# Kernel tuning notes

Hardware: AMD Instinct MI355X
Metric: run time of the kernel (lower is better)

Reference implementation:

```python
import jax, jax.numpy as jnp
import numpy as np
import math

SR = 24000
NH = 100      # num_harmonics
NF = 5        # num_formants
HID = 128
TWO_PI = 2.0 * math.pi


def conv1d(x, w, b, groups=1):
    # x: [B,C,T], w: [O, C//groups, K] (torch OIH layout), 'same' padding
    pad = (w.shape[-1] - 1) // 2
    y = jax.lax.conv_general_dilated(
        x, w, window_strides=(1,), padding=[(pad, pad)],
        dimension_numbers=('NCH', 'OIH', 'NCH'), feature_group_count=groups)
    return y + b[None, :, None]


def lrelu(x):
    return jnp.where(x >= 0, x, 0.1 * x)


def interp_linear(x, L):
    # torch F.interpolate(mode='linear', align_corners=False): x [B,C,T] -> [B,C,L]
    B, C, T = x.shape
    pos = (jnp.arange(L, dtype=x.dtype) + 0.5) * (T / L) - 0.5
    pos = jnp.clip(pos, 0.0, float(T - 1))
    lo = jnp.floor(pos).astype(jnp.int32)
    hi = jnp.minimum(lo + 1, T - 1)
    w = pos - lo.astype(x.dtype)
    return x[:, :, lo] * (1.0 - w) + x[:, :, hi] * w


def setup_inputs():
    key = jax.random.key(0)
    ks = jax.random.split(key, 30)
    ki = iter(range(30))
    def p(shape, s=0.05):
        return s * jax.random.normal(ks[next(ki)], shape, jnp.float32)
    B, T, L = 4, 500, 120000
    inp = {}
    # f0 in [80,120) Hz so actual_harmonics == num_harmonics (static shapes, see notes)
    inp['f0'] = 80.0 + 40.0 * jax.random.uniform(ks[next(ki)], (B, T), jnp.float32)
    inp['condition'] = jax.random.normal(ks[next(ki)], (B, HID, T), jnp.float32)
    # harmonic_amplitude_net params
    inp['ha_w1'] = p((HID, 1, 3));   inp['ha_b1'] = p((HID,))
    inp['ha_w2'] = p((256, HID, 1)); inp['ha_b2'] = p((256,))
    inp['ha_w3'] = p((256, 1, 3));   inp['ha_b3'] = p((256,))
    inp['ha_w4'] = p((256, 256, 1)); inp['ha_b4'] = p((256,))
    inp['ha_w5'] = p((NH, 256, 1));  inp['ha_b5'] = p((NH,))
    # formant predictor params
    inp['fm_w1'] = p((256, HID, 3));    inp['fm_b1'] = p((256,))
    inp['fm_w2'] = p((256, 256, 3));    inp['fm_b2'] = p((256,))
    inp['fm_w3'] = p((2 * NF, 256, 1)); inp['fm_b3'] = p((2 * NF,))
    # voice quality predictor params
    inp['vq_w1'] = p((128, HID, 3)); inp['vq_b1'] = p((128,))
    inp['vq_w2'] = p((64, 128, 3));  inp['vq_b2'] = p((64,))
    inp['vq_w3'] = p((3, 64, 1));    inp['vq_b3'] = p((3,))
    inp['audio_length'] = L
    return inp


def reference(f0, condition,
              ha_w1, ha_b1, ha_w2, ha_b2, ha_w3, ha_b3, ha_w4, ha_b4, ha_w5, ha_b5,
              fm_w1, fm_b1, fm_w2, fm_b2, fm_w3, fm_b3,
              vq_w1, vq_b1, vq_w2, vq_b2, vq_w3, vq_b3,
              audio_length):
    B, T = f0.shape
    L = audio_length
    # ---- harmonic_amplitude_net: (dw3 -> pw1 -> lrelu) x2 -> pw1 -> softplus ----
    a = lrelu(conv1d(conv1d(condition, ha_w1, ha_b1, groups=HID), ha_w2, ha_b2))
    a = lrelu(conv1d(conv1d(a, ha_w3, ha_b3, groups=256), ha_w4, ha_b4))
    harmonic_amplitudes = jax.nn.softplus(conv1d(a, ha_w5, ha_b5))  # [B,NH,T]
    # ---- FormantNetwork ----
    fp = conv1d(lrelu(conv1d(lrelu(conv1d(condition, fm_w1, fm_b1)), fm_w2, fm_b2)), fm_w3, fm_b3)
    ff = 200.0 + 3300.0 * jax.nn.sigmoid(fp[:, :NF])        # [B,NF,T]
    fbw = 50.0 + 150.0 * jax.nn.softplus(fp[:, NF:])        # [B,NF,T]
    hidx = jnp.arange(1, NH + 1, dtype=f0.dtype)
    hfreq = hidx[None, :, None] * f0[:, None, :]            # [B,NH,T]
    num = fbw ** 2                                          # [B,NF,T]
    den = (hfreq[:, None] - ff[:, :, None]) ** 2 + num[:, :, None]  # [B,NF,NH,T]
    res = num[:, :, None] / jnp.maximum(den, 1e-5)
    gain = jnp.prod(0.8 + 0.2 * res, axis=1)                # [B,NH,T]
    shaped = harmonic_amplitudes * gain
    # ---- VoiceQualityNetwork ----
    q = jax.nn.sigmoid(conv1d(lrelu(conv1d(lrelu(conv1d(condition, vq_w1, vq_b1)), vq_w2, vq_b2)), vq_w3, vq_b3))
    q_up = interp_linear(q, L)                              # [B,3,L]
    jitter = q_up[:, 0] * 0.05
    shimmer = q_up[:, 1] * 0.15
    breath = q_up[:, 2] * 0.3
    # ---- phase integration + harmonic bank ----
    f0_up = interp_linear(f0[:, None, :], L)[:, 0]          # [B,L]
    phase = jnp.cumsum(TWO_PI * f0_up / SR, axis=1)
    nk1, nk2, nk3 = jax.random.split(jax.random.key(42), 3)
    jphase = phase + jitter * jax.random.normal(nk1, phase.shape, phase.dtype)
    mask = (hidx[None, :, None] * f0_up[:, None, :] < SR / 2).astype(f0.dtype)  # [B,NH,L]
    amps_up = interp_linear(shaped, L)                      # [B,NH,L]
    sig = jnp.sum(amps_up * jnp.sin(jphase[:, None, :] * hidx[None, :, None]) * mask, axis=1)
    # ---- voice qualities: shimmer envelope + breath noise ----
    shim_env = 1.0 + jax.random.normal(nk2, sig.shape, sig.dtype) * shimmer
    out = sig * shim_env + jax.random.normal(nk3, sig.shape, sig.dtype) * breath
    return out
```

## Files before the change

### kernel.cpp

```cpp
#include <hip/hip_runtime.h>
#include <stdint.h>

#define B_ 4
#define T_ 500
#define L_ 120000
#define NH_ 100
#define N1_ 7500
#define N2_ 469
#define N2P_ 7504
#define N3_ 30
#define N3P_ 480
#define N4_ 2
#define N4P_ 32

#define ACT_NONE 0
#define ACT_LRELU 1
#define ACT_SOFTPLUS 2
#define ACT_SIGMOID 3

__host__ __device__ __forceinline__ uint32_t tf_rotl(uint32_t v, int d) {
  return (v << d) | (v >> (32 - d));
}
__host__ __device__ __forceinline__ void tf_block(uint32_t k0, uint32_t k1,
                                                  uint32_t& x0, uint32_t& x1) {
  uint32_t k2 = k0 ^ k1 ^ 0x1BD11BDAu;
  x0 += k0; x1 += k1;
#define TF_R(d) x0 += x1; x1 = tf_rotl(x1, (d)); x1 ^= x0;
  TF_R(13) TF_R(15) TF_R(26) TF_R(6)   x0 += k1; x1 += k2 + 1u;
  TF_R(17) TF_R(29) TF_R(16) TF_R(24)  x0 += k2; x1 += k0 + 2u;
  TF_R(13) TF_R(15) TF_R(26) TF_R(6)   x0 += k0; x1 += k1 + 3u;
  TF_R(17) TF_R(29) TF_R(16) TF_R(24)  x0 += k1; x1 += k2 + 4u;
  TF_R(13) TF_R(15) TF_R(26) TF_R(6)   x0 += k2; x1 += k0 + 5u;
#undef TF_R
}

__device__ __forceinline__ float erfinv_xla(float x) {
  float w = -log1pf(-(x * x));
  float p;
  if (w < 5.0f) {
    w = w - 2.5f;
    p = 2.81022636e-08f;
    p = fmaf(p, w, 3.43273939e-07f);
    p = fmaf(p, w, -3.5233877e-06f);
    p = fmaf(p, w, -4.39150654e-06f);
    p = fmaf(p, w, 0.00021858087f);
    p = fmaf(p, w, -0.00125372503f);
    p = fmaf(p, w, -0.00417768164f);
    p = fmaf(p, w, 0.246640727f);
    p = fmaf(p, w, 1.50140941f);
  } else {
    w = sqrtf(w) - 3.0f;
    p = -0.000200214257f;
    p = fmaf(p, w, 0.000100950558f);
    p = fmaf(p, w, 0.00134934322f);
    p = fmaf(p, w, -0.00367342844f);
    p = fmaf(p, w, 0.00573950773f);
    p = fmaf(p, w, -0.0076224613f);
    p = fmaf(p, w, 0.00943887047f);
    p = fmaf(p, w, 1.00167406f);
    p = fmaf(p, w, 2.83297682f);
  }
  return p * x;
}

__device__ __forceinline__ float jax_normal(uint32_t k0, uint32_t k1, uint32_t e) {
  uint32_t x0 = 0u, x1 = e;
  tf_block(k0, k1, x0, x1);
  uint32_t bits = x0 ^ x1;
  float u = __uint_as_float((bits >> 9) | 0x3f800000u) - 1.0f;
  float v = __fadd_rn(__fmul_rn(u, 2.0f), -0x1.fffffep-1f);
  v = fmaxf(v, -0x1.fffffep-1f);
  return __fmul_rn((float)1.4142135623730951, erfinv_xla(v));
}

__device__ __forceinline__ float sin_acc(float xf) {
  double x = (double)xf;
  double kd = rint(x * 6.3661977236758138e-01);
  double r = fma(-kd, 1.5707963267948966e+00, x);
  r = fma(-kd, 6.1232339957367660e-17, r);
  float rf = (float)r;
  float y = rf * rf;
  float ps = fmaf(y, 2.7557319e-06f, -1.9841270e-04f);
  ps = fmaf(y, ps, 8.3333335e-03f);
  ps = fmaf(y, ps, -0.16666667f);
  float s = fmaf(rf * y, ps, rf);
  float pc = fmaf(y, -2.7557319e-07f, 2.4801587e-05f);
  pc = fmaf(y, pc, -1.3888889e-03f);
  pc = fmaf(y, pc, 4.1666668e-02f);
  pc = fmaf(y, pc, -0.5f);
  float c = fmaf(y, pc, 1.0f);
  int q = ((int)kd) & 3;
  float rs = (q & 1) ? c : s;
  return (q & 2) ? -rs : rs;
}

__device__ __forceinline__ float apply_act(float v, int act) {
  switch (act) {
    case ACT_LRELU:    return v >= 0.0f ? v : 0.1f * v;
    case ACT_SOFTPLUS: return fmaxf(v, 0.0f) + log1pf(expf(-fabsf(v)));
    case ACT_SIGMOID:  return 1.0f / (1.0f + expf(-v));
  }
  return v;
}


__device__ __forceinline__ void conv3_path(
    const float* __restrict__ x, const float* __restrict__ w,
    const float* __restrict__ bias, float* __restrict__ y,
    int Cin, int Cout, int o0, int act, int b, int t0, float* smem) {
  float* sxf = smem;
  float* swf = smem + 64 * 68;
  int tid = threadIdx.x;
  int lane = tid & 63, og = tid >> 6;
  int t = t0 + lane;
  int o[4]; float acc[4];
#pragma unroll
  for (int i = 0; i < 4; ++i) {
    o[i] = o0 + 4 * og + i;
    acc[i] = (o[i] < Cout) ? bias[o[i]] : 0.0f;
  }
  float rx[17], rw[12];
  const int nch = Cin >> 6;
  auto ld = [&](int c) {
    int cb = c * 64;
#pragma unroll
    for (int k = 0; k < 17; ++k) {
      int idx = tid + 256 * k;
      int cc = idx / 68, j = idx - cc * 68;
      int tt = t0 - 1 + j;
      rx[k] = (j < 66 && tt >= 0 && tt < T_)
                  ? x[((size_t)b * Cin + cb + cc) * T_ + tt] : 0.0f;
    }
#pragma unroll
    for (int k = 0; k < 12; ++k) {
      int idx = tid + 256 * k;
      int oo = idx / 192, r = idx - oo * 192;
      rw[k] = (o0 + oo < Cout) ? w[((size_t)(o0 + oo) * Cin + cb) * 3 + r] : 0.0f;
    }
  };
  ld(0);
  for (int c = 0; c < nch; ++c) {
    __syncthreads();
#pragma unroll
    for (int k = 0; k < 17; ++k) sxf[tid + 256 * k] = rx[k];
#pragma unroll
    for (int k = 0; k < 12; ++k) {
      int idx = tid + 256 * k;
      int oo = idx / 192, r = idx - oo * 192;
      swf[(r / 3) * 52 + oo * 3 + (r % 3)] = rw[k];
    }
    __syncthreads();
    if (c + 1 < nch) ld(c + 1);
    for (int cc = 0; cc < 64; ++cc) {
      float xm  = sxf[cc * 68 + lane];
      float x0v = sxf[cc * 68 + lane + 1];
      float xp  = sxf[cc * 68 + lane + 2];
      const float4* wv4 = (const float4*)&swf[cc * 52 + og * 12];
      float4 wa = wv4[0], wb = wv4[1], wc = wv4[2];
      float wl[12] = {wa.x, wa.y, wa.z, wa.w, wb.x, wb.y, wb.z, wb.w,
                      wc.x, wc.y, wc.z, wc.w};
#pragma unroll
      for (int i = 0; i < 4; ++i) {
        acc[i] = fmaf(xm,  wl[3 * i + 0], acc[i]);
        acc[i] = fmaf(x0v, wl[3 * i + 1], acc[i]);
        acc[i] = fmaf(xp,  wl[3 * i + 2], acc[i]);
      }
    }
  }
  if (t < T_) {
#pragma unroll
    for (int i = 0; i < 4; ++i)
      if (o[i] < Cout) y[((size_t)b * Cout + o[i]) * T_ + t] = apply_act(acc[i], act);
  }
}

__device__ __forceinline__ void dwpw_path(
    const float* __restrict__ x, const float* __restrict__ wd,
    const float* __restrict__ bd, const float* __restrict__ wp,
    const float* __restrict__ bp, float* __restrict__ y,
    int Cin, int Cout, int o0, int act, int b, int t0, float* smem) {
  float* sxf  = smem;
  float* swdf = smem + 4352;
  float* swpf = smem + 4608;
  int tid = threadIdx.x;
  int lane = tid & 63, og = tid >> 6;
  int t = t0 + lane;
  int o[4]; float acc[4];
#pragma unroll
  for (int i = 0; i < 4; ++i) {
    o[i] = o0 + 4 * og + i;
    acc[i] = (o[i] < Cout) ? bp[o[i]] : 0.0f;
  }
  float rx[17], rwp[4], rwd1;
  const int nch = Cin >> 6;
  auto ld = [&](int c) {
    int cb = c * 64;
#pragma unroll
    for (int k = 0; k < 17; ++k) {
      int idx = tid + 256 * k;
      int cc = idx / 68, j = idx - cc * 68;
      int tt = t0 - 1 + j;
      rx[k] = (j < 66 && tt >= 0 && tt < T_)
                  ? x[((size_t)b * Cin + cb + cc) * T_ + tt] : 0.0f;
    }
    {
      int cc = tid >> 2, q = tid & 3;
      rwd1 = (q < 3) ? wd[(size_t)(cb + cc) * 3 + q] : bd[cb + cc];
    }
#pragma unroll
    for (int k = 0; k < 4; ++k) {
      int idx = tid + 256 * k;
      int oo = idx >> 6, cc = idx & 63;
      rwp[k] = (o0 + oo < Cout) ? wp[(size_t)(o0 + oo) * Cin + cb + cc] : 0.0f;
    }
  };
  ld(0);
  for (int c = 0; c < nch; ++c) {
    __syncthreads();
#pragma unroll
    for (int k = 0; k < 17; ++k) sxf[tid + 256 * k] = rx[k];
    swdf[tid] = rwd1;
#pragma unroll
    for (int k = 0; k < 4; ++k) {
      int idx = tid + 256 * k;
      int oo = idx >> 6, cc = idx & 63;
      swpf[cc * 20 + oo] = rwp[k];
    }
    __syncthreads();
    if (c + 1 < nch) ld(c + 1);
    float rd[16];
#pragma unroll
    for (int k = 0; k < 16; ++k) {
      int cc = og + 4 * k;
      rd[k] = fmaf(sxf[cc * 68 + lane], swdf[cc * 4 + 0],
              fmaf(sxf[cc * 68 + lane + 1], swdf[cc * 4 + 1],
              fmaf(sxf[cc * 68 + lane + 2], swdf[cc * 4 + 2], swdf[cc * 4 + 3])));
    }
    __syncthreads();
#pragma unroll
    for (int k = 0; k < 16; ++k) sxf[(og + 4 * k) * 64 + lane] = rd[k];
    __syncthreads();
    for (int cc = 0; cc < 64; ++cc) {
      float xv = sxf[cc * 64 + lane];
      float4 wv = *(const float4*)&swpf[cc * 20 + og * 4];
      acc[0] = fmaf(xv, wv.x, acc[0]);
      acc[1] = fmaf(xv, wv.y, acc[1]);
      acc[2] = fmaf(xv, wv.z, acc[2]);
      acc[3] = fmaf(xv, wv.w, acc[3]);
    }
  }
  if (t < T_) {
#pragma unroll
    for (int i = 0; i < 4; ++i)
      if (o[i] < Cout) y[((size_t)b * Cout + o[i]) * T_ + t] = apply_act(acc[i], act);
  }
}

__device__ __forceinline__ void pw_path(
    const float* __restrict__ x, const float* __restrict__ w,
    const float* __restrict__ bias, float* __restrict__ y,
    int Cin, int Cout, int o0, int act, int b, int t0, float* smem) {
  float* sxf = smem;
  float* swf = smem + 4096;
  int tid = threadIdx.x;
  int lane = tid & 63, og = tid >> 6;
  int t = t0 + lane;
  int o[4]; float acc[4];
#pragma unroll
  for (int i = 0; i < 4; ++i) {
    o[i] = o0 + 4 * og + i;
    acc[i] = (o[i] < Cout) ? bias[o[i]] : 0.0f;
  }
  float rx[16], rw[4];
  const int nch = Cin >> 6;
  auto ld = [&](int c) {
    int cb = c * 64;
#pragma unroll
    for (int k = 0; k < 16; ++k) {
      int idx = tid + 256 * k;
      int cc = idx >> 6, j = idx & 63;
      int tt = t0 + j;
      rx[k] = (tt < T_) ? x[((size_t)b * Cin + cb + cc) * T_ + tt] : 0.0f;
    }
#pragma unroll
    for (int k = 0; k < 4; ++k) {
      int idx = tid + 256 * k;
      int oo = idx >> 6, cc = idx & 63;
      rw[k] = (o0 + oo < Cout) ? w[(size_t)(o0 + oo) * Cin + cb + cc] : 0.0f;
    }
  };
  ld(0);
  for (int c = 0; c < nch; ++c) {
    __syncthreads();
#pragma unroll
    for (int k = 0; k < 16; ++k) sxf[tid + 256 * k] = rx[k];
#pragma unroll
    for (int k = 0; k < 4; ++k) {
      int idx = tid + 256 * k;
      int oo = idx >> 6, cc = idx & 63;
      swf[cc * 20 + oo] = rw[k];
    }
    __syncthreads();
    if (c + 1 < nch) ld(c + 1);
    for (int cc = 0; cc < 64; ++cc) {
      float xv = sxf[cc * 64 + lane];
      float4 wv = *(const float4*)&swf[cc * 20 + og * 4];
      acc[0] = fmaf(xv, wv.x, acc[0]);
      acc[1] = fmaf(xv, wv.y, acc[1]);
      acc[2] = fmaf(xv, wv.z, acc[2]);
      acc[3] = fmaf(xv, wv.w, acc[3]);
    }
  }
  if (t < T_) {
#pragma unroll
    for (int i = 0; i < 4; ++i)
      if (o[i] < Cout) y[((size_t)b * Cout + o[i]) * T_ + t] = apply_act(acc[i], act);
  }
}

__device__ void rwr_body(const float* __restrict__ A1, float* __restrict__ A2,
                         float* __restrict__ A3, float* __restrict__ A4,
                         float* __restrict__ E5, float* __restrict__ E3o,
                         float* __restrict__ E2o) {
  int tid = threadIdx.x;
  for (int gid = tid; gid < B_ * N2_; gid += 256) {
    int b = gid / N2_, w = gid - b * N2_;
    float S = 0.0f;
    for (int m = 0; m < 16; ++m) {
      int i = w * 16 + m;
      float v = (i < N1_) ? A1[(size_t)b * L_ + (size_t)i * 16 + 15] : 0.0f;
      S = __fadd_rn(S, v);
      A2[(size_t)b * N2P_ + i] = S;
    }
  }
  __syncthreads();
  for (int gid = tid; gid < B_ * N3_; gid += 256) {
    int b = gid / N3_, w = gid - b * N3_;
    float S = 0.0f;
    for (int m = 0; m < 16; ++m) {
      int i = w * 16 + m;
      float v = (i < N2_) ? A2[(size_t)b * N2P_ + (size_t)i * 16 + 15] : 0.0f;
      S = __fadd_rn(S, v);
      A3[(size_t)b * N3P_ + i] = S;
    }
  }
  __syncthreads();
  for (int gid = tid; gid < B_ * N4_; gid += 256) {
    int b = gid / N4_, w = gid - b * N4_;
    float S = 0.0f;
    for (int m = 0; m < 16; ++m) {
      int i = w * 16 + m;
      float v = (i < N3_) ? A3[(size_t)b * N3P_ + (size_t)i * 16 + 15] : 0.0f;
      S = __fadd_rn(S, v);
      A4[(size_t)b * N4P_ + i] = S;
    }
  }
  __syncthreads();
  if (tid < B_) {
    E5[tid * N4_ + 0] = 0.0f;
    E5[tid * N4_ + 1] = A4[(size_t)tid * N4P_ + 15];
  }
  __syncthreads();
  for (int gid = tid; gid < B_ * N3_; gid += 256) {
    int b = gid / N3_, k = gid - b * N3_;
    float v = 0.0f;
    if (k > 0) {
      int i = k - 1;
      v = __fadd_rn(E5[b * N4_ + (i >> 4)], A4[(size_t)b * N4P_ + i]);
    }
    E3o[b * N3_ + k] = v;
  }
  __syncthreads();
  for (int gid = tid; gid < B_ * N2_; gid += 256) {
    int b = gid / N2_, j = gid - b * N2_;
    float v = 0.0f;
    if (j > 0) {
      int i = j - 1;
      v = __fadd_rn(E3o[b * N3_ + (i >> 4)], A3[(size_t)b * N3P_ + i]);
    }
    E2o[b * N2_ + j] = v;
  }
}

__global__ void __launch_bounds__(256) conv_l1(
    const float* __restrict__ cond,
    const float* __restrict__ fw1, const float* __restrict__ fb1,
    const float* __restrict__ vw1, const float* __restrict__ vb1,
    const float* __restrict__ hw1, const float* __restrict__ hb1,
    const float* __restrict__ hw2, const float* __restrict__ hb2,
    float* __restrict__ fmA, float* __restrict__ vqB, float* __restrict__ haB,
    const float* __restrict__ A1, float* __restrict__ A2, float* __restrict__ A3,
    float* __restrict__ A4, float* __restrict__ E5, float* __restrict__ E3o,
    float* __restrict__ E2o) {
  __shared__ __align__(16) float smem[7680];
  int yy = blockIdx.y, b = blockIdx.z, t0 = blockIdx.x * 64;
  if (yy < 16) {
    conv3_path(cond, fw1, fb1, fmA, 128, 256, yy * 16, ACT_LRELU, b, t0, smem);
  } else if (yy < 24) {
    conv3_path(cond, vw1, vb1, vqB, 128, 128, (yy - 16) * 16, ACT_LRELU, b, t0, smem);
  } else if (yy < 40) {
    dwpw_path(cond, hw1, hb1, hw2, hb2, haB, 128, 256, (yy - 24) * 16, ACT_LRELU, b, t0, smem);
  } else {
    if (blockIdx.x != 0 || blockIdx.z != 0) return;
    rwr_body(A1, A2, A3, A4, E5, E3o, E2o);
  }
}

__global__ void __launch_bounds__(256) conv_l2(
    const float* __restrict__ fmA, const float* __restrict__ vqB,
    const float* __restrict__ haB,
    const float* __restrict__ fw2, const float* __restrict__ fb2,
    const float* __restrict__ vw2, const float* __restrict__ vb2,
    const float* __restrict__ hw3, const float* __restrict__ hb3,
    const float* __restrict__ hw4, const float* __restrict__ hb4,
    float* __restrict__ fmC, float* __restrict__ vqC, float* __restrict__ haC) {
  __shared__ __align__(16) float smem[7680];
  int yy = blockIdx.y, b = blockIdx.z, t0 = blockIdx.x * 64;
  if (yy < 16) {
    conv3_path(fmA, fw2, fb2, fmC, 256, 256, yy * 16, ACT_LRELU, b, t0, smem);
  } else if (yy < 20) {
    conv3_path(vqB, vw2, vb2, vqC, 128, 64, (yy - 16) * 16, ACT_LRELU, b, t0, smem);
  } else {
    dwpw_path(haB, hw3, hb3, hw4, hb4, haC, 256, 256, (yy - 20) * 16, ACT_LRELU, b, t0, smem);
  }
}

__global__ void __launch_bounds__(256) conv_l3(
    const float* __restrict__ haC, const float* __restrict__ fmC,
    const float* __restrict__ vqC,
    const float* __restrict__ hw5, const float* __restrict__ hb5,
    const float* __restrict__ fw3, const float* __restrict__ fb3,
    const float* __restrict__ vw3, const float* __restrict__ vb3,
    float* __restrict__ ha, float* __restrict__ fp, float* __restrict__ qv) {
  __shared__ __align__(16) float smem[5376];
  int yy = blockIdx.y, b = blockIdx.z, t0 = blockIdx.x * 64;
  if (yy < 7) {
    pw_path(haC, hw5, hb5, ha, 256, 100, yy * 16, ACT_SOFTPLUS, b, t0, smem);
  } else if (yy == 7) {
    pw_path(fmC, fw3, fb3, fp, 256, 10, 0, ACT_NONE, b, t0, smem);
  } else {
    pw_path(vqC, vw3, vb3, qv, 64, 3, 0, ACT_SIGMOID, b, t0, smem);
  }
}

__global__ void shaped_kernel(const float* __restrict__ ha, const float* __restrict__ fp,
                              const float* __restrict__ f0, float* __restrict__ out) {
  int t = blockIdx.x, b = blockIdx.y, h = threadIdx.x;
  __shared__ float ff[5], nm[5];
  if (h < 10) {
    float v = fp[((size_t)b * 10 + h) * T_ + t];
    if (h < 5) {
      ff[h] = 200.0f + 3300.0f * (1.0f / (1.0f + expf(-v)));
    } else {
      float bw = 50.0f + 150.0f * (fmaxf(v, 0.0f) + log1pf(expf(-fabsf(v))));
      nm[h - 5] = bw * bw;
    }
  }
  __syncthreads();
  if (h >= NH_) return;
  float hfreq = (float)(h + 1) * f0[(size_t)b * T_ + t];
  float g = 1.0f;
  for (int i = 0; i < 5; ++i) {
    float d = hfreq - ff[i];
    float den = d * d + nm[i];
    float res = nm[i] / fmaxf(den, 1e-5f);
    g = g * (0.8f + 0.2f * res);
  }
  out[((size_t)b * NH_ + h) * T_ + t] = ha[((size_t)b * NH_ + h) * T_ + t] * g;
}

__global__ void terms_l1(const float* __restrict__ f0, float* __restrict__ A1) {
  int gid = blockIdx.x * blockDim.x + threadIdx.x;
  if (gid >= B_ * N1_) return;
  int b = gid / N1_, w = gid - b * N1_;
  const float* f0b = f0 + (size_t)b * T_;
  float* a = A1 + (size_t)b * L_ + (size_t)w * 16;
  const float RINV = (float)(500.0 / 120000.0);
  float S = 0.0f;
  int lbase = w * 16;
  for (int i = 0; i < 16; ++i) {
    int l = lbase + i;
    float pos = __fsub_rn(__fmul_rn(__fadd_rn((float)l, 0.5f), RINV), 0.5f);
    pos = fminf(fmaxf(pos, 0.0f), 499.0f);
    int lo = (int)floorf(pos);
    int hi = lo + 1; hi = hi < (T_ - 1) ? hi : (T_ - 1);
    float wt = __fsub_rn(pos, (float)lo);
    float omw = __fsub_rn(1.0f, wt);
    float f0up = __fadd_rn(__fmul_rn(f0b[lo], omw), __fmul_rn(f0b[hi], wt));
    float trm = __fdiv_rn(__fmul_rn((float)6.283185307179586, f0up), 24000.0f);
    S = __fadd_rn(S, trm);
    a[i] = S;
  }
}

__global__ void __launch_bounds__(256) main_kernel(
    const float* __restrict__ A1, const float* __restrict__ A2,
    const float* __restrict__ E2o,
    const float* __restrict__ shaped, const float* __restrict__ q,
    const float* __restrict__ f0, float* __restrict__ out,
    uint32_t k10, uint32_t k11, uint32_t k20, uint32_t k21, uint32_t k30, uint32_t k31) {
  const float RINV = (float)(500.0 / 120000.0);
  int b = blockIdx.y;
  int l0 = blockIdx.x * 256;
  int l = l0 + threadIdx.x;
  __shared__ float ls[4][NH_];
  float p0 = __fsub_rn(__fmul_rn(__fadd_rn((float)l0, 0.5f), RINV), 0.5f);
  p0 = fminf(fmaxf(p0, 0.0f), 499.0f);
  int lo0 = (int)floorf(p0);
  for (int i = threadIdx.x; i < 4 * NH_; i += 256) {
    int j = i / NH_, h = i - j * NH_;
    int col = lo0 + j; col = col < (T_ - 1) ? col : (T_ - 1);
    ls[j][h] = shaped[((size_t)b * NH_ + h) * T_ + col];
  }
  __syncthreads();
  if (l >= L_) return;

  float pos = __fsub_rn(__fmul_rn(__fadd_rn((float)l, 0.5f), RINV), 0.5f);
  pos = fminf(fmaxf(pos, 0.0f), 499.0f);
  int lo = (int)floorf(pos);
  int hi = lo + 1; hi = hi < (T_ - 1) ? hi : (T_ - 1);
  float w = __fsub_rn(pos, (float)lo);
  float omw = __fsub_rn(1.0f, w);

  const float* f0b = f0 + (size_t)b * T_;
  float f0up = __fadd_rn(__fmul_rn(f0b[lo], omw), __fmul_rn(f0b[hi], w));
  const float* qb = q + (size_t)b * 3 * T_;
  float q0 = __fadd_rn(__fmul_rn(qb[lo], omw), __fmul_rn(qb[hi], w));
  float q1 = __fadd_rn(__fmul_rn(qb[T_ + lo], omw), __fmul_rn(qb[T_ + hi], w));
  float q2 = __fadd_rn(__fmul_rn(qb[2 * T_ + lo], omw), __fmul_rn(qb[2 * T_ + hi], w));
  float jit = __fmul_rn(q0, 0.05f);
  float shm = __fmul_rn(q1, 0.15f);
  float brt = __fmul_rn(q2, 0.3f);

  uint32_t e = (uint32_t)(b * L_ + l);
  float n1 = jax_normal(k10, k11, e);
  float n2 = jax_normal(k20, k21, e);
  float n3 = jax_normal(k30, k31, e);

  float e1v = 0.0f;
  int r = l >> 4;
  if (r > 0) {
    int i = r - 1;
    e1v = __fadd_rn(E2o[b * N2_ + (i >> 4)], A2[(size_t)b * N2P_ + i]);
  }
  float phf = __fadd_rn(e1v, A1[(size_t)b * L_ + l]);
  float jph = __fadd_rn(phf, __fmul_rn(jit, n1));

  int jlo = lo - lo0;
  int jhi = hi - lo0; jhi = jhi < 3 ? jhi : 3;

  float acc = 0.0f;
  for (int h = 1; h <= NH_; ++h) {
    float amp = __fadd_rn(__fmul_rn(ls[jlo][h - 1], omw), __fmul_rn(ls[jhi][h - 1], w));
    float hf = (float)h;
    float arg = __fmul_rn(jph, hf);
    float s = sin_acc(arg);
    float m = (__fmul_rn(hf, f0up) < 12000.0f) ? 1.0f : 0.0f;
    acc = __fadd_rn(acc, __fmul_rn(__fmul_rn(amp, s), m));
  }
  float env = __fadd_rn(1.0f, __fmul_rn(n2, shm));
  out[(size_t)b * L_ + l] = __fadd_rn(__fmul_rn(acc, env), __fmul_rn(n3, brt));
}

extern "C" void kernel_launch(void* const* d_in, const int* in_sizes, int n_in,
                              void* d_out, int out_size, void* d_ws, size_t ws_size,
                              hipStream_t stream) {
  const float* f0    = (const float*)d_in[0];
  const float* cond  = (const float*)d_in[1];
  const float* ha_w1 = (const float*)d_in[2];
  const float* ha_b1 = (const float*)d_in[3];
  const float* ha_w2 = (const float*)d_in[4];
  const float* ha_b2 = (const float*)d_in[5];
  const float* ha_w3 = (const float*)d_in[6];
  const float* ha_b3 = (const float*)d_in[7];
  const float* ha_w4 = (const float*)d_in[8];
  const float* ha_b4 = (const float*)d_in[9];
  const float* ha_w5 = (const float*)d_in[10];
  const float* ha_b5 = (const float*)d_in[11];
  const float* fm_w1 = (const float*)d_in[12];
  const float* fm_b1 = (const float*)d_in[13];
  const float* fm_w2 = (const float*)d_in[14];
  const float* fm_b2 = (const float*)d_in[15];
  const float* fm_w3 = (const float*)d_in[16];
  const float* fm_b3 = (const float*)d_in[17];
  const float* vq_w1 = (const float*)d_in[18];
  const float* vq_b1 = (const float*)d_in[19];
  const float* vq_w2 = (const float*)d_in[20];
  const float* vq_b2 = (const float*)d_in[21];
  const float* vq_w3 = (const float*)d_in[22];
  const float* vq_b3 = (const float*)d_in[23];
  float* out = (float*)d_out;

  uint32_t kw[3][2];
  for (uint32_t j = 0; j < 3; ++j) {
    uint32_t x0 = 0u, x1 = j;
    tf_block(0u, 42u, x0, x1);
    kw[j][0] = x0; kw[j][1] = x1;
  }

  float* ws = (float*)d_ws;
  size_t off = 0;
  auto take = [&](size_t n) { float* p = ws + off; off += (n + 3) & ~(size_t)3; return p; };
  float* fmA = take(512000);
  float* haB = take(512000);
  float* fmC = take(512000);
  float* haC = take(512000);
  float* vqB = take(256000);
  float* vqC = take(128000);
  float* A1  = take((size_t)B_ * L_);
  float* A2  = take((size_t)B_ * N2P_);
  float* A3  = take((size_t)B_ * N3P_);
  float* A4  = take((size_t)B_ * N4P_);
  float* E5  = take((size_t)B_ * N4_);
  float* E3o = take((size_t)B_ * N3_);
  float* E2o = take((size_t)B_ * N2_);
  float* ha = fmA;
  float* fp = vqB;
  float* qv = vqB + 20480;
  float* sh = haB;

  terms_l1<<<(B_ * N1_ + 255) / 256, 256, 0, stream>>>(f0, A1);
  conv_l1<<<dim3(8, 41, B_), 256, 0, stream>>>(
      cond, fm_w1, fm_b1, vq_w1, vq_b1, ha_w1, ha_b1, ha_w2, ha_b2,
      fmA, vqB, haB, A1, A2, A3, A4, E5, E3o, E2o);
  conv_l2<<<dim3(8, 36, B_), 256, 0, stream>>>(
      fmA, vqB, haB, fm_w2, fm_b2, vq_w2, vq_b2, ha_w3, ha_b3, ha_w4, ha_b4,
      fmC, vqC, haC);
  conv_l3<<<dim3(8, 9, B_), 256, 0, stream>>>(
      haC, fmC, vqC, ha_w5, ha_b5, fm_w3, fm_b3, vq_w3, vq_b3, ha, fp, qv);
  shaped_kernel<<<dim3(T_, B_), 128, 0, stream>>>(ha, fp, f0, sh);
  main_kernel<<<dim3((L_ + 255) / 256, B_), 256, 0, stream>>>(
      A1, A2, E2o, sh, qv, f0, out,
      kw[0][0], kw[0][1], kw[1][0], kw[1][1], kw[2][0], kw[2][1]);
  (void)in_sizes; (void)n_in; (void)out_size; (void)ws_size;
}
```

Baseline: 296.3 us.

## Retile conv paths to 2 timesteps x 8 channels per thread with wider time tiles

The three conv helper paths are restructured so each thread computes 2 adjacent timesteps for 8 output channels, using float2/float4 shared-memory loads. Time tiles grow from 64 to 256 (or 128 for pointwise) and channel chunks shrink from 64 to 32, which raises register-level reuse of inputs and weights. The grids shrink to match, and the serial rwr_body work moves from conv_l1 into conv_l2. The trade-off is far fewer blocks per launch, which may underfill the GPU, plus higher register pressure.

New measurement: 293.3 us. No clear change (-1.0%).

```diff
diff --git a/kernel.cpp b/kernel.cpp
--- a/kernel.cpp
+++ b/kernel.cpp
@@ -17,6 +17,8 @@
 #define ACT_LRELU 1
 #define ACT_SOFTPLUS 2
 #define ACT_SIGMOID 3
+
+#define SXW 268
 
 __host__ __device__ __forceinline__ uint32_t tf_rotl(uint32_t v, int d) {
   return (v << d) | (v >> (32 - d));
@@ -109,32 +111,36 @@
     const float* __restrict__ bias, float* __restrict__ y,
     int Cin, int Cout, int o0, int act, int b, int t0, float* smem) {
   float* sxf = smem;
-  float* swf = smem + 64 * 68;
+  float* swf = smem + 32 * SXW;
   int tid = threadIdx.x;
-  int lane = tid & 63, og = tid >> 6;
-  int t = t0 + lane;
-  int o[4]; float acc[4];
-#pragma unroll
-  for (int i = 0; i < 4; ++i) {
-    o[i] = o0 + 4 * og + i;
-    acc[i] = (o[i] < Cout) ? bias[o[i]] : 0.0f;
-  }
-  float rx[17], rw[12];
-  const int nch = Cin >> 6;
+  int lane = tid & 63;
+  int wid = tid >> 6;
+  int og = wid & 1, th = wid >> 1;
+  int tl = th * 128 + 2 * lane;
+  int t = t0 + tl;
+  int obase = o0 + og * 8;
+  float acc[8][2];
+#pragma unroll
+  for (int i = 0; i < 8; ++i) {
+    float bv = (obase + i < Cout) ? bias[obase + i] : 0.0f;
+    acc[i][0] = bv; acc[i][1] = bv;
+  }
+  float rx[33], rw[6];
+  const int nch = Cin >> 5;
   auto ld = [&](int c) {
-    int cb = c * 64;
-#pragma unroll
-    for (int k = 0; k < 17; ++k) {
-      int idx = tid + 256 * k;
-      int cc = idx / 68, j = idx - cc * 68;
+    int cb = c * 32;
+#pragma unroll
+    for (int k = 0; k < 33; ++k) {
+      int idx = tid + 256 * k;
+      int cc = idx / 258, j = idx - cc * 258;
       int tt = t0 - 1 + j;
-      rx[k] = (j < 66 && tt >= 0 && tt < T_)
+      rx[k] = (idx < 8256 && tt >= 0 && tt < T_)
                   ? x[((size_t)b * Cin + cb + cc) * T_ + tt] : 0.0f;
     }
 #pragma unroll
-    for (int k = 0; k < 12; ++k) {
-      int idx = tid + 256 * k;
-      int oo = idx / 192, r = idx - oo * 192;
+    for (int k = 0; k < 6; ++k) {
+      int idx = tid + 256 * k;
+      int oo = idx / 96, r = idx - oo * 96;
       rw[k] = (o0 + oo < Cout) ? w[((size_t)(o0 + oo) * Cin + cb) * 3 + r] : 0.0f;
     }
   };
@@ -142,35 +148,49 @@
   for (int c = 0; c < nch; ++c) {
     __syncthreads();
 #pragma unroll
-    for (int k = 0; k < 17; ++k) sxf[tid + 256 * k] = rx[k];
-#pragma unroll
-    for (int k = 0; k < 12; ++k) {
-      int idx = tid + 256 * k;
-      int oo = idx / 192, r = idx - oo * 192;
+    for (int k = 0; k < 33; ++k) {
+      int idx = tid + 256 * k;
+      if (idx < 8256) {
+        int cc = idx / 258, j = idx - cc * 258;
+        sxf[cc * SXW + j] = rx[k];
+      }
+    }
+#pragma unroll
+    for (int k = 0; k < 6; ++k) {
+      int idx = tid + 256 * k;
+      int oo = idx / 96, r = idx - oo * 96;
       swf[(r / 3) * 52 + oo * 3 + (r % 3)] = rw[k];
     }
     __syncthreads();
     if (c + 1 < nch) ld(c + 1);
-    for (int cc = 0; cc < 64; ++cc) {
-      float xm  = sxf[cc * 68 + lane];
-      float x0v = sxf[cc * 68 + lane + 1];
-      float xp  = sxf[cc * 68 + lane + 2];
-      const float4* wv4 = (const float4*)&swf[cc * 52 + og * 12];
-      float4 wa = wv4[0], wb = wv4[1], wc = wv4[2];
-      float wl[12] = {wa.x, wa.y, wa.z, wa.w, wb.x, wb.y, wb.z, wb.w,
-                      wc.x, wc.y, wc.z, wc.w};
-#pragma unroll
-      for (int i = 0; i < 4; ++i) {
-        acc[i] = fmaf(xm,  wl[3 * i + 0], acc[i]);
-        acc[i] = fmaf(x0v, wl[3 * i + 1], acc[i]);
-        acc[i] = fmaf(xp,  wl[3 * i + 2], acc[i]);
+    for (int cc = 0; cc < 32; ++cc) {
+      const float* row = sxf + cc * SXW + tl;
+      float2 xa = *(const float2*)row;
+      float2 xb = *(const float2*)(row + 2);
+      const float4* wq = (const float4*)(swf + cc * 52 + og * 24);
+      float4 wA = wq[0], wB = wq[1], wC = wq[2], wD = wq[3], wE = wq[4], wF = wq[5];
+      float wl[24] = {wA.x, wA.y, wA.z, wA.w, wB.x, wB.y, wB.z, wB.w,
+                      wC.x, wC.y, wC.z, wC.w, wD.x, wD.y, wD.z, wD.w,
+                      wE.x, wE.y, wE.z, wE.w, wF.x, wF.y, wF.z, wF.w};
+#pragma unroll
+      for (int i = 0; i < 8; ++i) {
+        float w0 = wl[3 * i], w1 = wl[3 * i + 1], w2 = wl[3 * i + 2];
+        acc[i][0] = fmaf(xa.x, w0, acc[i][0]);
+        acc[i][0] = fmaf(xa.y, w1, acc[i][0]);
+        acc[i][0] = fmaf(xb.x, w2, acc[i][0]);
+        acc[i][1] = fmaf(xa.y, w0, acc[i][1]);
+        acc[i][1] = fmaf(xb.x, w1, acc[i][1]);
+        acc[i][1] = fmaf(xb.y, w2, acc[i][1]);
       }
     }
   }
-  if (t < T_) {
-#pragma unroll
-    for (int i = 0; i < 4; ++i)
-      if (o[i] < Cout) y[((size_t)b * Cout + o[i]) * T_ + t] = apply_act(acc[i], act);
+#pragma unroll
+  for (int i = 0; i < 8; ++i) {
+    int o = obase + i;
+    if (o < Cout) {
+      if (t < T_)     y[((size_t)b * Cout + o) * T_ + t]     = apply_act(acc[i][0], act);
+      if (t + 1 < T_) y[((size_t)b * Cout + o) * T_ + t + 1] = apply_act(acc[i][1], act);
+    }
   }
 }
 
@@ -180,37 +200,41 @@
     const float* __restrict__ bp, float* __restrict__ y,
     int Cin, int Cout, int o0, int act, int b, int t0, float* smem) {
   float* sxf  = smem;
-  float* swdf = smem + 4352;
-  float* swpf = smem + 4608;
+  float* swdf = smem + 32 * SXW;
+  float* swpf = swdf + 128;
   int tid = threadIdx.x;
-  int lane = tid & 63, og = tid >> 6;
-  int t = t0 + lane;
-  int o[4]; float acc[4];
-#pragma unroll
-  for (int i = 0; i < 4; ++i) {
-    o[i] = o0 + 4 * og + i;
-    acc[i] = (o[i] < Cout) ? bp[o[i]] : 0.0f;
-  }
-  float rx[17], rwp[4], rwd1;
-  const int nch = Cin >> 6;
+  int lane = tid & 63;
+  int wid = tid >> 6;
+  int og = wid & 1, th = wid >> 1;
+  int tl = th * 128 + 2 * lane;
+  int t = t0 + tl;
+  int obase = o0 + og * 8;
+  float acc[8][2];
+#pragma unroll
+  for (int i = 0; i < 8; ++i) {
+    float bv = (obase + i < Cout) ? bp[obase + i] : 0.0f;
+    acc[i][0] = bv; acc[i][1] = bv;
+  }
+  float rx[33], rwp[2], rwd1 = 0.0f;
+  const int nch = Cin >> 5;
   auto ld = [&](int c) {
-    int cb = c * 64;
-#pragma unroll
-    for (int k = 0; k < 17; ++k) {
-      int idx = tid + 256 * k;
-      int cc = idx / 68, j = idx - cc * 68;
+    int cb = c * 32;
+#pragma unroll
+    for (int k = 0; k < 33; ++k) {
+      int idx = tid + 256 * k;
+      int cc = idx / 258, j = idx - cc * 258;
       int tt = t0 - 1 + j;
-      rx[k] = (j < 66 && tt >= 0 && tt < T_)
+      rx[k] = (idx < 8256 && tt >= 0 && tt < T_)
                   ? x[((size_t)b * Cin + cb + cc) * T_ + tt] : 0.0f;
     }
-    {
+    if (tid < 128) {
       int cc = tid >> 2, q = tid & 3;
       rwd1 = (q < 3) ? wd[(size_t)(cb + cc) * 3 + q] : bd[cb + cc];
     }
 #pragma unroll
-    for (int k = 0; k < 4; ++k) {
-      int idx = tid + 256 * k;
-      int oo = idx >> 6, cc = idx & 63;
+    for (int k = 0; k < 2; ++k) {
+      int idx = tid + 256 * k;
+      int oo = idx >> 5, cc = idx & 31;
       rwp[k] = (o0 + oo < Cout) ? wp[(size_t)(o0 + oo) * Cin + cb + cc] : 0.0f;
     }
   };
@@ -218,41 +242,65 @@
   for (int c = 0; c < nch; ++c) {
     __syncthreads();
 #pragma unroll
-    for (int k = 0; k < 17; ++k) sxf[tid + 256 * k] = rx[k];
-    swdf[tid] = rwd1;
-#pragma unroll
-    for (int k = 0; k < 4; ++k) {
-      int idx = tid + 256 * k;
-      int oo = idx >> 6, cc = idx & 63;
+    for (int k = 0; k < 33; ++k) {
+      int idx = tid + 256 * k;
+      if (idx < 8256) {
+        int cc = idx / 258, j = idx - cc * 258;
+        sxf[cc * SXW + j] = rx[k];
+      }
+    }
+    if (tid < 128) swdf[tid] = rwd1;
+#pragma unroll
+    for (int k = 0; k < 2; ++k) {
+      int idx = tid + 256 * k;
+      int oo = idx >> 5, cc = idx & 31;
       swpf[cc * 20 + oo] = rwp[k];
+    }
+    __syncthreads();
+    {
+      int ccd = tid & 31, tseg = tid >> 5;
+      const float* row = sxf + ccd * SXW + tseg * 32;
+      float dw0 = swdf[ccd * 4 + 0], dw1 = swdf[ccd * 4 + 1];
+      float dw2 = swdf[ccd * 4 + 2], dw3 = swdf[ccd * 4 + 3];
+      float rd[32];
+      float4 va = *(const float4*)row;
+#pragma unroll
+      for (int m = 0; m < 8; ++m) {
+        float4 vb = *(const float4*)(row + 4 * m + 4);
+        rd[4 * m + 0] = fmaf(va.x, dw0, fmaf(va.y, dw1, fmaf(va.z, dw2, dw3)));
+        rd[4 * m + 1] = fmaf(va.y, dw0, fmaf(va.z, dw1, fmaf(va.w, dw2, dw3)));
+        rd[4 * m + 2] = fmaf(va.z, dw0, fmaf(va.w, dw1, fmaf(vb.x, dw2, dw3)));
+        rd[4 * m + 3] = fmaf(va.w, dw0, fmaf(vb.x, dw1, fmaf(vb.y, dw2, dw3)));
+        va = vb;
+      }
+      __syncthreads();
+      float* drow = sxf + ccd * SXW + tseg * 32;
+#pragma unroll
+      for (int m = 0; m < 8; ++m)
+        *(float4*)(drow + 4 * m) =
+            make_float4(rd[4 * m], rd[4 * m + 1], rd[4 * m + 2], rd[4 * m + 3]);
     }
     __syncthreads();
     if (c + 1 < nch) ld(c + 1);
-    float rd[16];
-#pragma unroll
-    for (int k = 0; k < 16; ++k) {
-      int cc = og + 4 * k;
-      rd[k] = fmaf(sxf[cc * 68 + lane], swdf[cc * 4 + 0],
-              fmaf(sxf[cc * 68 + lane + 1], swdf[cc * 4 + 1],
-              fmaf(sxf[cc * 68 + lane + 2], swdf[cc * 4 + 2], swdf[cc * 4 + 3])));
-    }
-    __syncthreads();
-#pragma unroll
-    for (int k = 0; k < 16; ++k) sxf[(og + 4 * k) * 64 + lane] = rd[k];
-    __syncthreads();
-    for (int cc = 0; cc < 64; ++cc) {
-      float xv = sxf[cc * 64 + lane];
-      float4 wv = *(const float4*)&swpf[cc * 20 + og * 4];
-      acc[0] = fmaf(xv, wv.x, acc[0]);
-      acc[1] = fmaf(xv, wv.y, acc[1]);
-      acc[2] = fmaf(xv, wv.z, acc[2]);
-      acc[3] = fmaf(xv, wv.w, acc[3]);
-    }
-  }
-  if (t < T_) {
-#pragma unroll
-    for (int i = 0; i < 4; ++i)
-      if (o[i] < Cout) y[((size_t)b * Cout + o[i]) * T_ + t] = apply_act(acc[i], act);
+    for (int cc = 0; cc < 32; ++cc) {
+      float2 xv = *(const float2*)(sxf + cc * SXW + tl);
+      const float4* wq = (const float4*)(swpf + cc * 20 + og * 8);
+      float4 wA = wq[0], wB = wq[1];
+      float wl[8] = {wA.x, wA.y, wA.z, wA.w, wB.x, wB.y, wB.z, wB.w};
+#pragma unroll
+      for (int i = 0; i < 8; ++i) {
+        acc[i][0] = fmaf(xv.x, wl[i], acc[i][0]);
+        acc[i][1] = fmaf(xv.y, wl[i], acc[i][1]);
+      }
+    }
+  }
+#pragma unroll
+  for (int i = 0; i < 8; ++i) {
+    int o = obase + i;
+    if (o < Cout) {
+      if (t < T_)     y[((size_t)b * Cout + o) * T_ + t]     = apply_act(acc[i][0], act);
+      if (t + 1 < T_) y[((size_t)b * Cout + o) * T_ + t + 1] = apply_act(acc[i][1], act);
+    }
   }
 }
 
@@ -261,31 +309,34 @@
     const float* __restrict__ bias, float* __restrict__ y,
     int Cin, int Cout, int o0, int act, int b, int t0, float* smem) {
   float* sxf = smem;
-  float* swf = smem + 4096;
+  float* swf = smem + 32 * 128;
   int tid = threadIdx.x;
-  int lane = tid & 63, og = tid >> 6;
-  int t = t0 + lane;
-  int o[4]; float acc[4];
-#pragma unroll
-  for (int i = 0; i < 4; ++i) {
-    o[i] = o0 + 4 * og + i;
-    acc[i] = (o[i] < Cout) ? bias[o[i]] : 0.0f;
+  int lane = tid & 63;
+  int og = tid >> 6;
+  int tl = 2 * lane;
+  int t = t0 + tl;
+  int obase = o0 + og * 8;
+  float acc[8][2];
+#pragma unroll
+  for (int i = 0; i < 8; ++i) {
+    float bv = (obase + i < Cout) ? bias[obase + i] : 0.0f;
+    acc[i][0] = bv; acc[i][1] = bv;
   }
   float rx[16], rw[4];
-  const int nch = Cin >> 6;
+  const int nch = Cin >> 5;
   auto ld = [&](int c) {
-    int cb = c * 64;
+    int cb = c * 32;
 #pragma unroll
     for (int k = 0; k < 16; ++k) {
       int idx = tid + 256 * k;
-      int cc = idx >> 6, j = idx & 63;
+      int cc = idx >> 7, j = idx & 127;
       int tt = t0 + j;
       rx[k] = (tt < T_) ? x[((size_t)b * Cin + cb + cc) * T_ + tt] : 0.0f;
     }
 #pragma unroll
     for (int k = 0; k < 4; ++k) {
       int idx = tid + 256 * k;
-      int oo = idx >> 6, cc = idx & 63;
+      int oo = idx >> 5, cc = idx & 31;
       rw[k] = (o0 + oo < Cout) ? w[(size_t)(o0 + oo) * Cin + cb + cc] : 0.0f;
     }
   };
@@ -293,28 +344,38 @@
   for (int c = 0; c < nch; ++c) {
     __syncthreads();
 #pragma unroll
-    for (int k = 0; k < 16; ++k) sxf[tid + 256 * k] = rx[k];
+    for (int k = 0; k < 16; ++k) {
+      int idx = tid + 256 * k;
+      int cc = idx >> 7, j = idx & 127;
+      sxf[cc * 128 + j] = rx[k];
+    }
 #pragma unroll
     for (int k = 0; k < 4; ++k) {
       int idx = tid + 256 * k;
-      int oo = idx >> 6, cc = idx & 63;
-      swf[cc * 20 + oo] = rw[k];
+      int oo = idx >> 5, cc = idx & 31;
+      swf[cc * 36 + oo] = rw[k];
     }
     __syncthreads();
     if (c + 1 < nch) ld(c + 1);
-    for (int cc = 0; cc < 64; ++cc) {
-      float xv = sxf[cc * 64 + lane];
-      float4 wv = *(const float4*)&swf[cc * 20 + og * 4];
-      acc[0] = fmaf(xv, wv.x, acc[0]);
-      acc[1] = fmaf(xv, wv.y, acc[1]);
-      acc[2] = fmaf(xv, wv.z, acc[2]);
-      acc[3] = fmaf(xv, wv.w, acc[3]);
-    }
-  }
-  if (t < T_) {
-#pragma unroll
-    for (int i = 0; i < 4; ++i)
-      if (o[i] < Cout) y[((size_t)b * Cout + o[i]) * T_ + t] = apply_act(acc[i], act);
+    for (int cc = 0; cc < 32; ++cc) {
+      float2 xv = *(const float2*)(sxf + cc * 128 + tl);
+      const float4* wq = (const float4*)(swf + cc * 36 + og * 8);
+      float4 wA = wq[0], wB = wq[1];
+      float wl[8] = {wA.x, wA.y, wA.z, wA.w, wB.x, wB.y, wB.z, wB.w};
+#pragma unroll
+      for (int i = 0; i < 8; ++i) {
+        acc[i][0] = fmaf(xv.x, wl[i], acc[i][0]);
+        acc[i][1] = fmaf(xv.y, wl[i], acc[i][1]);
+      }
+    }
+  }
+#pragma unroll
+  for (int i = 0; i < 8; ++i) {
+    int o = obase + i;
+    if (o < Cout) {
+      if (t < T_)     y[((size_t)b * Cout + o) * T_ + t]     = apply_act(acc[i][0], act);
+      if (t + 1 < T_) y[((size_t)b * Cout + o) * T_ + t + 1] = apply_act(acc[i][1], act);
+    }
   }
 }
 
@@ -388,21 +449,15 @@
     const float* __restrict__ vw1, const float* __restrict__ vb1,
     const float* __restrict__ hw1, const float* __restrict__ hb1,
     const float* __restrict__ hw2, const float* __restrict__ hb2,
-    float* __restrict__ fmA, float* __restrict__ vqB, float* __restrict__ haB,
-    const float* __restrict__ A1, float* __restrict__ A2, float* __restrict__ A3,
-    float* __restrict__ A4, float* __restrict__ E5, float* __restrict__ E3o,
-    float* __restrict__ E2o) {
-  __shared__ __align__(16) float smem[7680];
-  int yy = blockIdx.y, b = blockIdx.z, t0 = blockIdx.x * 64;
+    float* __restrict__ fmA, float* __restrict__ vqB, float* __restrict__ haB) {
+  __shared__ __align__(16) float smem[32 * SXW + 32 * 52];
+  int yy = blockIdx.y, b = blockIdx.z, t0 = blockIdx.x * 256;
   if (yy < 16) {
     conv3_path(cond, fw1, fb1, fmA, 128, 256, yy * 16, ACT_LRELU, b, t0, smem);
   } else if (yy < 24) {
     conv3_path(cond, vw1, vb1, vqB, 128, 128, (yy - 16) * 16, ACT_LRELU, b, t0, smem);
-  } else if (yy < 40) {
+  } else {
     dwpw_path(cond, hw1, hb1, hw2, hb2, haB, 128, 256, (yy - 24) * 16, ACT_LRELU, b, t0, smem);
-  } else {
-    if (blockIdx.x != 0 || blockIdx.z != 0) return;
-    rwr_body(A1, A2, A3, A4, E5, E3o, E2o);
   }
 }
 
@@ -413,15 +468,21 @@
     const float* __restrict__ vw2, const float* __restrict__ vb2,
     const float* __restrict__ hw3, const float* __restrict__ hb3,
     const float* __restrict__ hw4, const float* __restrict__ hb4,
-    float* __restrict__ fmC, float* __restrict__ vqC, float* __restrict__ haC) {
-  __shared__ __align__(16) float smem[7680];
-  int yy = blockIdx.y, b = blockIdx.z, t0 = blockIdx.x * 64;
+    float* __restrict__ fmC, float* __restrict__ vqC, float* __restrict__ haC,
+    const float* __restrict__ A1, float* __restrict__ A2, float* __restrict__ A3,
+    float* __restrict__ A4, float* __restrict__ E5, float* __restrict__ E3o,
+    float* __restrict__ E2o) {
+  __shared__ __align__(16) float smem[32 * SXW + 32 * 52];
+  int yy = blockIdx.y, b = blockIdx.z, t0 = blockIdx.x * 256;
   if (yy < 16) {
     conv3_path(fmA, fw2, fb2, fmC, 256, 256, yy * 16, ACT_LRELU, b, t0, smem);
   } else if (yy < 20) {
     conv3_path(vqB, vw2, vb2, vqC, 128, 64, (yy - 16) * 16, ACT_LRELU, b, t0, smem);
+  } else if (yy < 36) {
+    dwpw_path(haB, hw3, hb3, hw4, hb4, haC, 256, 256, (yy - 20) * 16, ACT_LRELU, b, t0, smem);
   } else {
-    dwpw_path(haB, hw3, hb3, hw4, hb4, haC, 256, 256, (yy - 20) * 16, ACT_LRELU, b, t0, smem);
+    if (blockIdx.x != 0 || blockIdx.z != 0) return;
+    rwr_body(A1, A2, A3, A4, E5, E3o, E2o);
   }
 }
 
@@ -432,11 +493,11 @@
     const float* __restrict__ fw3, const float* __restrict__ fb3,
     const float* __restrict__ vw3, const float* __restrict__ vb3,
     float* __restrict__ ha, float* __restrict__ fp, float* __restrict__ qv) {
-  __shared__ __align__(16) float smem[5376];
-  int yy = blockIdx.y, b = blockIdx.z, t0 = blockIdx.x * 64;
-  if (yy < 7) {
-    pw_path(haC, hw5, hb5, ha, 256, 100, yy * 16, ACT_SOFTPLUS, b, t0, smem);
-  } else if (yy == 7) {
+  __shared__ __align__(16) float smem[32 * 128 + 32 * 36];
+  int yy = blockIdx.y, b = blockIdx.z, t0 = blockIdx.x * 128;
+  if (yy < 4) {
+    pw_path(haC, hw5, hb5, ha, 256, 100, yy * 32, ACT_SOFTPLUS, b, t0, smem);
+  } else if (yy == 4) {
     pw_path(fmC, fw3, fb3, fp, 256, 10, 0, ACT_NONE, b, t0, smem);
   } else {
     pw_path(vqC, vw3, vb3, qv, 64, 3, 0, ACT_SIGMOID, b, t0, smem);
@@ -620,13 +681,13 @@
   float* sh = haB;
 
   terms_l1<<<(B_ * N1_ + 255) / 256, 256, 0, stream>>>(f0, A1);
-  conv_l1<<<dim3(8, 41, B_), 256, 0, stream>>>(
+  conv_l1<<<dim3(2, 40, B_), 256, 0, stream>>>(
       cond, fm_w1, fm_b1, vq_w1, vq_b1, ha_w1, ha_b1, ha_w2, ha_b2,
-      fmA, vqB, haB, A1, A2, A3, A4, E5, E3o, E2o);
-  conv_l2<<<dim3(8, 36, B_), 256, 0, stream>>>(
+      fmA, vqB, haB);
+  conv_l2<<<dim3(2, 37, B_), 256, 0, stream>>>(
       fmA, vqB, haB, fm_w2, fm_b2, vq_w2, vq_b2, ha_w3, ha_b3, ha_w4, ha_b4,
-      fmC, vqC, haC);
-  conv_l3<<<dim3(8, 9, B_), 256, 0, stream>>>(
+      fmC, vqC, haC, A1, A2, A3, A4, E5, E3o, E2o);
+  conv_l3<<<dim3(4, 6, B_), 256, 0, stream>>>(
       haC, fmC, vqC, ha_w5, ha_b5, fm_w3, fm_b3, vq_w3, vq_b3, ha, fp, qv);
   shaped_kernel<<<dim3(T_, B_), 128, 0, stream>>>(ha, fp, f0, sh);
   main_kernel<<<dim3((L_ + 255) / 256, B_), 256, 0, stream>>>(
```
